# Optimization experiments

Measured on AMD Instinct MI355X. Metric: run time of the kernel, lower is better.

Reference implementation:

```python
import jax, jax.numpy as jnp
import numpy as np

NPOINTS = 1024


def setup_inputs() -> dict:
    key = jax.random.key(0)
    B, N, C = 64, 131072, 3
    pos = jax.random.normal(key, (B, N, C), dtype=jnp.float32)
    return {"pos": pos, "start_idx": 0}


def reference(pos, start_idx):
    """Farthest point sampling. pos: (B, N, C) -> indices (B, NPOINTS) int32."""
    B, N, C = pos.shape
    start = jnp.full((B,), start_idx, dtype=jnp.int32)
    dist0 = jnp.full((B, N), jnp.inf, dtype=pos.dtype)

    def step(carry, _):
        dist, last = carry                                   # dist: (B,N), last: (B,)
        last_pos = jnp.take_along_axis(pos, last[:, None, None], axis=1)  # (B,1,C)
        d = jnp.sum((pos - last_pos) ** 2, axis=-1)          # (B,N) squared dist to newest sample
        dist = jnp.minimum(dist, d)                          # min to-sample-set distance
        nxt = jnp.argmax(dist, axis=-1).astype(jnp.int32)    # farthest point
        return (dist, nxt), last                             # emit index selected this step

    (_, _), idxs = jax.lax.scan(step, (dist0, start), None, length=NPOINTS)
    return idxs.T  # (B, NPOINTS); first column == start_idx
```

## Files before the change

### kernel.cpp

```cpp
#include <hip/hip_runtime.h>
#include <stdint.h>

#define NB    64
#define NN    131072
#define NPTS  1024
#define TPB   512
#define WPB   4
#define NWAVE (TPB / 64)
#define CHUNK (NN / WPB)
#define PPT   (CHUNK / TPB)
#define RPTS  40
#define LPTS  24
#define RPAIR (RPTS / 2)
#define LPAIR (LPTS / 2)

typedef float v2f __attribute__((ext_vector_type(2)));
typedef unsigned long long u64;

static __device__ __forceinline__ v2f vmin2(v2f a, v2f b) {
#if __has_builtin(__builtin_elementwise_min)
    return __builtin_elementwise_min(a, b);
#else
    v2f r; r.x = fminf(a.x, b.x); r.y = fminf(a.y, b.y); return r;
#endif
}


__global__ __launch_bounds__(TPB)
__attribute__((amdgpu_waves_per_eu(2, 2)))
void fps_kernel(
    const float* __restrict__ pos,
    const int*   __restrict__ start_p,
    int*         __restrict__ out,
    u64*         __restrict__ slots)
{
#pragma clang fp contract(off)
    const int wg   = blockIdx.x;
    const int xcd  = wg & 7;
    const int sl   = wg >> 3;
    const int b    = xcd * 8 + (sl >> 2);
    const int r    = sl & 3;
    const int t    = threadIdx.x;
    const int lane = t & 63;
    const int wv   = t >> 6;

    const float* __restrict__ P  = pos + (size_t)b * NN * 3;
    const float* __restrict__ Pc = P + (size_t)r * CHUNK * 3;
    u64* __restrict__ bslots = slots + (size_t)b * NPTS * WPB;

    __shared__ float lx[LPAIR * TPB * 2];
    __shared__ float ly[LPAIR * TPB * 2];
    __shared__ float lz[LPAIR * TPB * 2];
    __shared__ u64   wred[2][NWAVE];

    v2f rx[RPAIR], ry[RPAIR], rz[RPAIR];
#pragma unroll
    for (int p = 0; p < RPAIR; ++p) {
        const float* a = Pc + (size_t)(t + (2 * p) * TPB) * 3;
        const float* c = a + (size_t)TPB * 3;
        rx[p] = (v2f){a[0], c[0]};
        ry[p] = (v2f){a[1], c[1]};
        rz[p] = (v2f){a[2], c[2]};
    }
#pragma unroll
    for (int l = 0; l < LPAIR; ++l) {
        const float* a = Pc + (size_t)(t + (RPTS + 2 * l) * TPB) * 3;
        const float* c = a + (size_t)TPB * 3;
        const int idx = (l * TPB + t) * 2;
        lx[idx] = a[0]; lx[idx + 1] = c[0];
        ly[idx] = a[1]; ly[idx + 1] = c[1];
        lz[idx] = a[2]; lz[idx + 1] = c[2];
    }

    const int start = start_p[0];
    float sx = P[(size_t)start * 3 + 0];
    float sy = P[(size_t)start * 3 + 1];
    float sz = P[(size_t)start * 3 + 2];
    if (r == 0 && t == 0) out[(size_t)b * NPTS] = start;

    v2f dist[PPT / 2];
#pragma unroll
    for (int p = 0; p < PPT / 2; ++p)
        dist[p] = (v2f){__builtin_inff(), __builtin_inff()};

    const int gbase = r * CHUNK;

    for (int k = 1; k < NPTS; ++k) {
        const int bank = k & 1;
        const v2f s0 = (v2f){sx, sx}, s1 = (v2f){sy, sy}, s2 = (v2f){sz, sz};
        float best = -1.0f;
        int   bi   = 0;

#define PAIR_STEP(DP, PX, PY, PZ, I0)                                    \
        {                                                                \
            v2f dx = (PX) - s0, dy = (PY) - s1, dz = (PZ) - s2;          \
            v2f d  = (dx * dx + dy * dy) + dz * dz;                      \
            v2f nd = vmin2(dist[DP], d);                                 \
            dist[DP] = nd;                                               \
            if (nd.x > best) { best = nd.x; bi = (I0); }                 \
            if (nd.y > best) { best = nd.y; bi = (I0) + TPB; }           \
        }

#pragma unroll
        for (int p = 0; p < RPAIR; ++p)
            PAIR_STEP(p, rx[p], ry[p], rz[p], gbase + t + (2 * p) * TPB);
#pragma unroll
        for (int l = 0; l < LPAIR; ++l) {
            const int idx = (l * TPB + t) * 2;
            v2f px = *reinterpret_cast<const v2f*>(&lx[idx]);
            v2f py = *reinterpret_cast<const v2f*>(&ly[idx]);
            v2f pz = *reinterpret_cast<const v2f*>(&lz[idx]);
            PAIR_STEP(RPAIR + l, px, py, pz, gbase + t + (RPTS + 2 * l) * TPB);
        }
#undef PAIR_STEP

        u64 pk = ((u64)__float_as_uint(best) << 32) | (unsigned)~bi;

#pragma unroll
        for (int o = 32; o >= 1; o >>= 1) {
            u64 q = __shfl_xor(pk, o, 64);
            if (q > pk) pk = q;
        }
        if (lane == 0) wred[bank][wv] = pk;
        __syncthreads();

        u64 v = wred[bank][lane & (NWAVE - 1)];
#pragma unroll
        for (int o = 1; o < NWAVE; o <<= 1) {
            u64 q = __shfl_xor(v, o, 64);
            if (q > v) v = q;
        }
        if (t == 0)
            __hip_atomic_store(&bslots[(size_t)k * WPB + r], v,
                               __ATOMIC_RELAXED, __HIP_MEMORY_SCOPE_AGENT);

        const u64* sp = &bslots[(size_t)k * WPB + (lane & 3)];
        u64 g;
        for (;;) {
            g = __hip_atomic_load(sp, __ATOMIC_RELAXED, __HIP_MEMORY_SCOPE_AGENT);
            if (g) break;
            __builtin_amdgcn_s_sleep(1);
        }
#pragma unroll
        for (int o = 1; o <= 2; o <<= 1) {
            u64 q = __shfl_xor(g, o, 64);
            if (q > g) g = q;
        }
        const int widx = (int)~(unsigned)g;
        if (r == 0 && t == 0) out[(size_t)b * NPTS + k] = widx;
        sx = P[(size_t)widx * 3 + 0];
        sy = P[(size_t)widx * 3 + 1];
        sz = P[(size_t)widx * 3 + 2];
    }
}

extern "C" void kernel_launch(void* const* d_in, const int* in_sizes, int n_in,
                              void* d_out, int out_size, void* d_ws, size_t ws_size,
                              hipStream_t stream)
{
    const float* pos     = (const float*)d_in[0];
    const int*   start_p = (const int*)d_in[1];
    int*         out     = (int*)d_out;
    u64*         slots   = (u64*)d_ws;

    hipMemsetAsync(d_ws, 0, (size_t)NB * NPTS * WPB * sizeof(u64), stream);

    void* args[] = { (void*)&pos, (void*)&start_p, (void*)&out, (void*)&slots };
    hipError_t e = hipLaunchCooperativeKernel((const void*)fps_kernel,
                                              dim3(NB * WPB), dim3(TPB),
                                              args, 0, stream);
    if (e != hipSuccess) {
        fps_kernel<<<dim3(NB * WPB), dim3(TPB), 0, stream>>>(pos, start_p, out, slots);
    }
}
```

Measured before the change: 4.003 ms.

## Publish winner coordinates through slots and use vectorized max-then-index argmax

```diff
diff --git a/kernel.cpp b/kernel.cpp
--- a/kernel.cpp
+++ b/kernel.cpp
@@ -13,6 +13,7 @@
 #define LPTS  24
 #define RPAIR (RPTS / 2)
 #define LPAIR (LPTS / 2)
+#define NPAIR (PPT / 2)
 
 typedef float v2f __attribute__((ext_vector_type(2)));
 typedef unsigned long long u64;
@@ -24,8 +25,16 @@
     v2f r; r.x = fminf(a.x, b.x); r.y = fminf(a.y, b.y); return r;
 #endif
 }
-
-
+static __device__ __forceinline__ v2f vmax2(v2f a, v2f b) {
+#if __has_builtin(__builtin_elementwise_max)
+    return __builtin_elementwise_max(a, b);
+#else
+    v2f r; r.x = fmaxf(a.x, b.x); r.y = fmaxf(a.y, b.y); return r;
+#endif
+}
+
+
+template <bool PAYLOAD>
 __global__ __launch_bounds__(TPB)
 __attribute__((amdgpu_waves_per_eu(2, 2)))
 void fps_kernel(
@@ -46,7 +55,8 @@
 
     const float* __restrict__ P  = pos + (size_t)b * NN * 3;
     const float* __restrict__ Pc = P + (size_t)r * CHUNK * 3;
-    u64* __restrict__ bslots = slots + (size_t)b * NPTS * WPB;
+    u64* __restrict__ bslots = slots +
+        (PAYLOAD ? (size_t)b * NPTS * WPB * 4 : (size_t)b * NPTS * WPB);
 
     __shared__ float lx[LPAIR * TPB * 2];
     __shared__ float ly[LPAIR * TPB * 2];
@@ -78,50 +88,81 @@
     float sz = P[(size_t)start * 3 + 2];
     if (r == 0 && t == 0) out[(size_t)b * NPTS] = start;
 
-    v2f dist[PPT / 2];
-#pragma unroll
-    for (int p = 0; p < PPT / 2; ++p)
+    v2f dist[NPAIR];
+#pragma unroll
+    for (int p = 0; p < NPAIR; ++p)
         dist[p] = (v2f){__builtin_inff(), __builtin_inff()};
 
     const int gbase = r * CHUNK;
+    const unsigned bt = (unsigned)(gbase + t);
 
     for (int k = 1; k < NPTS; ++k) {
         const int bank = k & 1;
         const v2f s0 = (v2f){sx, sx}, s1 = (v2f){sy, sy}, s2 = (v2f){sz, sz};
-        float best = -1.0f;
-        int   bi   = 0;
-
-#define PAIR_STEP(DP, PX, PY, PZ, I0)                                    \
+
+        v2f vb[4];
+#pragma unroll
+        for (int q = 0; q < 4; ++q) vb[q] = (v2f){-1.0f, -1.0f};
+
+#define PAIR_STEP(DP, PX, PY, PZ)                                        \
         {                                                                \
             v2f dx = (PX) - s0, dy = (PY) - s1, dz = (PZ) - s2;          \
             v2f d  = (dx * dx + dy * dy) + dz * dz;                      \
             v2f nd = vmin2(dist[DP], d);                                 \
             dist[DP] = nd;                                               \
-            if (nd.x > best) { best = nd.x; bi = (I0); }                 \
-            if (nd.y > best) { best = nd.y; bi = (I0) + TPB; }           \
+            vb[(DP) >> 3] = vmax2(vb[(DP) >> 3], nd);                    \
         }
 
 #pragma unroll
         for (int p = 0; p < RPAIR; ++p)
-            PAIR_STEP(p, rx[p], ry[p], rz[p], gbase + t + (2 * p) * TPB);
+            PAIR_STEP(p, rx[p], ry[p], rz[p]);
 #pragma unroll
         for (int l = 0; l < LPAIR; ++l) {
             const int idx = (l * TPB + t) * 2;
             v2f px = *reinterpret_cast<const v2f*>(&lx[idx]);
             v2f py = *reinterpret_cast<const v2f*>(&ly[idx]);
             v2f pz = *reinterpret_cast<const v2f*>(&lz[idx]);
-            PAIR_STEP(RPAIR + l, px, py, pz, gbase + t + (RPTS + 2 * l) * TPB);
+            PAIR_STEP(RPAIR + l, px, py, pz);
         }
 #undef PAIR_STEP
 
-        u64 pk = ((u64)__float_as_uint(best) << 32) | (unsigned)~bi;
-
+        float m[4];
+#pragma unroll
+        for (int q = 0; q < 4; ++q) m[q] = fmaxf(vb[q].x, vb[q].y);
+        float wbest = fmaxf(fmaxf(m[0], m[1]), fmaxf(m[2], m[3]));
+#pragma unroll
+        for (int o = 32; o >= 1; o >>= 1)
+            wbest = fmaxf(wbest, __shfl_xor(wbest, o, 64));
+
+        unsigned biL = 0xFFFFFFFFu;
+#pragma unroll
+        for (int q = 0; q < 4; ++q) {
+            if (__any(m[q] == wbest)) {
+#pragma unroll
+                for (int p = 8 * q; p < 8 * q + 8; ++p) {
+                    if (dist[p].x == wbest)
+                        biL = min(biL, bt + (unsigned)((2 * p) * TPB));
+                    if (dist[p].y == wbest)
+                        biL = min(biL, bt + (unsigned)((2 * p + 1) * TPB));
+                }
+            }
+        }
+
+        unsigned bw = biL;
 #pragma unroll
         for (int o = 32; o >= 1; o >>= 1) {
-            u64 q = __shfl_xor(pk, o, 64);
-            if (q > pk) pk = q;
-        }
-        if (lane == 0) wred[bank][wv] = pk;
+            unsigned q = (unsigned)__shfl_xor((int)bw, o, 64);
+            bw = min(bw, q);
+        }
+
+        u64 wkey;
+        if (PAYLOAD)
+            wkey = ((u64)__float_as_uint(wbest) << 32) |
+                   ((u64)(NN - 1 - bw) << 10) | (unsigned)k;
+        else
+            wkey = ((u64)__float_as_uint(wbest) << 32) | (unsigned)~bw;
+
+        if (lane == 0) wred[bank][wv] = wkey;
         __syncthreads();
 
         u64 v = wred[bank][lane & (NWAVE - 1)];
@@ -130,27 +171,86 @@
             u64 q = __shfl_xor(v, o, 64);
             if (q > v) v = q;
         }
-        if (t == 0)
-            __hip_atomic_store(&bslots[(size_t)k * WPB + r], v,
-                               __ATOMIC_RELAXED, __HIP_MEMORY_SCOPE_AGENT);
-
-        const u64* sp = &bslots[(size_t)k * WPB + (lane & 3)];
-        u64 g;
-        for (;;) {
-            g = __hip_atomic_load(sp, __ATOMIC_RELAXED, __HIP_MEMORY_SCOPE_AGENT);
-            if (g) break;
-            __builtin_amdgcn_s_sleep(1);
-        }
-#pragma unroll
-        for (int o = 1; o <= 2; o <<= 1) {
-            u64 q = __shfl_xor(g, o, 64);
-            if (q > g) g = q;
-        }
-        const int widx = (int)~(unsigned)g;
-        if (r == 0 && t == 0) out[(size_t)b * NPTS + k] = widx;
-        sx = P[(size_t)widx * 3 + 0];
-        sy = P[(size_t)widx * 3 + 1];
-        sz = P[(size_t)widx * 3 + 2];
+
+        if (PAYLOAD) {
+            const unsigned cwidx = NN - 1 - (unsigned)((v >> 10) & 0x1FFFFull);
+            if (biL == cwidx) {
+                u64* sb = bslots + ((size_t)k * WPB + r) * 4;
+                __hip_atomic_store(sb + 3, v, __ATOMIC_RELAXED, __HIP_MEMORY_SCOPE_AGENT);
+                const unsigned jj = (cwidx - bt) >> 9;
+                float wx, wy, wz;
+                if (jj >= RPTS) {
+                    const int jl  = (int)jj - RPTS;
+                    const int idx = ((jl >> 1) * TPB + t) * 2 + (jl & 1);
+                    wx = lx[idx]; wy = ly[idx]; wz = lz[idx];
+                } else {
+                    const float* a = Pc + (size_t)(t + jj * TPB) * 3;
+                    wx = a[0]; wy = a[1]; wz = a[2];
+                }
+                const u64 kk = (u64)(unsigned)k;
+                __hip_atomic_store(sb + 0, ((u64)__float_as_uint(wx) << 32) | kk,
+                                   __ATOMIC_RELAXED, __HIP_MEMORY_SCOPE_AGENT);
+                __hip_atomic_store(sb + 1, ((u64)__float_as_uint(wy) << 32) | kk,
+                                   __ATOMIC_RELAXED, __HIP_MEMORY_SCOPE_AGENT);
+                __hip_atomic_store(sb + 2, ((u64)__float_as_uint(wz) << 32) | kk,
+                                   __ATOMIC_RELAXED, __HIP_MEMORY_SCOPE_AGENT);
+            }
+
+            const u64* sp = bslots + ((size_t)k * WPB + (lane & 3)) * 4;
+            u64 g3;
+            for (;;) {
+                g3 = __hip_atomic_load(sp + 3, __ATOMIC_RELAXED, __HIP_MEMORY_SCOPE_AGENT);
+                if ((unsigned)(g3 & 1023ull) == (unsigned)k) break;
+                __builtin_amdgcn_s_sleep(1);
+            }
+#pragma unroll
+            for (int o = 1; o <= 2; o <<= 1) {
+                u64 q = __shfl_xor(g3, o, 64);
+                if (q > g3) g3 = q;
+            }
+            const int widx = NN - 1 - (int)((g3 >> 10) & 0x1FFFFull);
+            if (r == 0 && t == 0) out[(size_t)b * NPTS + k] = widx;
+
+            const u64* wp = bslots + ((size_t)k * WPB + (widx >> 15)) * 4;
+            u64 c0, c1, c2;
+            for (;;) {
+                c0 = __hip_atomic_load(wp + 0, __ATOMIC_RELAXED, __HIP_MEMORY_SCOPE_AGENT);
+                if ((unsigned)c0 == (unsigned)k) break;
+                __builtin_amdgcn_s_sleep(1);
+            }
+            for (;;) {
+                c1 = __hip_atomic_load(wp + 1, __ATOMIC_RELAXED, __HIP_MEMORY_SCOPE_AGENT);
+                if ((unsigned)c1 == (unsigned)k) break;
+            }
+            for (;;) {
+                c2 = __hip_atomic_load(wp + 2, __ATOMIC_RELAXED, __HIP_MEMORY_SCOPE_AGENT);
+                if ((unsigned)c2 == (unsigned)k) break;
+            }
+            sx = __uint_as_float((unsigned)(c0 >> 32));
+            sy = __uint_as_float((unsigned)(c1 >> 32));
+            sz = __uint_as_float((unsigned)(c2 >> 32));
+        } else {
+            if (t == 0)
+                __hip_atomic_store(&bslots[(size_t)k * WPB + r], v,
+                                   __ATOMIC_RELAXED, __HIP_MEMORY_SCOPE_AGENT);
+            const u64* sp = &bslots[(size_t)k * WPB + (lane & 3)];
+            u64 g;
+            for (;;) {
+                g = __hip_atomic_load(sp, __ATOMIC_RELAXED, __HIP_MEMORY_SCOPE_AGENT);
+                if (g) break;
+                __builtin_amdgcn_s_sleep(1);
+            }
+#pragma unroll
+            for (int o = 1; o <= 2; o <<= 1) {
+                u64 q = __shfl_xor(g, o, 64);
+                if (q > g) g = q;
+            }
+            const int widx = (int)~(unsigned)g;
+            if (r == 0 && t == 0) out[(size_t)b * NPTS + k] = widx;
+            sx = P[(size_t)widx * 3 + 0];
+            sy = P[(size_t)widx * 3 + 1];
+            sz = P[(size_t)widx * 3 + 2];
+        }
     }
 }
 
@@ -163,13 +263,26 @@
     int*         out     = (int*)d_out;
     u64*         slots   = (u64*)d_ws;
 
-    hipMemsetAsync(d_ws, 0, (size_t)NB * NPTS * WPB * sizeof(u64), stream);
+    const size_t needP = (size_t)NB * NPTS * WPB * 4 * sizeof(u64);
+    const size_t need1 = (size_t)NB * NPTS * WPB * sizeof(u64);
 
     void* args[] = { (void*)&pos, (void*)&start_p, (void*)&out, (void*)&slots };
-    hipError_t e = hipLaunchCooperativeKernel((const void*)fps_kernel,
-                                              dim3(NB * WPB), dim3(TPB),
-                                              args, 0, stream);
-    if (e != hipSuccess) {
-        fps_kernel<<<dim3(NB * WPB), dim3(TPB), 0, stream>>>(pos, start_p, out, slots);
-    }
-}
+
+    if (ws_size >= needP) {
+        hipMemsetAsync(d_ws, 0, needP, stream);
+        hipError_t e = hipLaunchCooperativeKernel(
+            (const void*)fps_kernel<true>, dim3(NB * WPB), dim3(TPB),
+            args, 0, stream);
+        if (e != hipSuccess)
+            fps_kernel<true><<<dim3(NB * WPB), dim3(TPB), 0, stream>>>(
+                pos, start_p, out, slots);
+    } else {
+        hipMemsetAsync(d_ws, 0, need1, stream);
+        hipError_t e = hipLaunchCooperativeKernel(
+            (const void*)fps_kernel<false>, dim3(NB * WPB), dim3(TPB),
+            args, 0, stream);
+        if (e != hipSuccess)
+            fps_kernel<false><<<dim3(NB * WPB), dim3(TPB), 0, stream>>>(
+                pos, start_p, out, slots);
+    }
+}
```

Measured after the change: 4.552 ms. 1.14x slower.
